# Kernel tuning notes

Measured on AMD Instinct MI355X. Metric: run time of the kernel, lower is better.

The kernel has to match this reference:

```python
import jax, jax.numpy as jnp
import numpy as np

#   x_out = Dy(alpha) @ J @ Dy(beta) @ J @ Dy(gamma) @ x   (per-irrep block diagonal)
# Dy(theta) is the sparse cos/sin y-rotation (exactly what encode_rotation_angle feeds
# into the segmented tensor product), and J = D(rotation by pi about (x+y)/sqrt(2)) is
# the constant Wigner matrix that conjugates a y-rotation into an x-rotation.

LMAX = 8
MUL = 64
LS = list(range(LMAX + 1))
DIM = MUL * sum(2 * l + 1 for l in LS)  # 5184
BATCH = 16384


def _so3_generators(l):
    # real antisymmetric so(3) generators for degree l (e3nn/cuE convention)
    m = np.arange(-l, l)
    raising = np.diag(-np.sqrt(l * (l + 1) - m * (m + 1)), k=-1).astype(np.complex128)
    m = np.arange(-l + 1, l + 1)
    lowering = np.diag(np.sqrt(l * (l + 1) - m * (m - 1)), k=1).astype(np.complex128)
    m = np.arange(-l, l + 1)
    X = np.stack([0.5 * (raising + lowering), np.diag(1j * m).astype(np.complex128),
                  -0.5j * (raising - lowering)])
    # change of basis complex -> real spherical harmonics
    q = np.zeros((2 * l + 1, 2 * l + 1), dtype=np.complex128)
    for mm in range(-l, 0):
        q[l + mm, l + abs(mm)] = 1.0 / np.sqrt(2)
        q[l + mm, l - abs(mm)] = -1j / np.sqrt(2)
    q[l, l] = 1.0
    for mm in range(1, l + 1):
        q[l + mm, l + abs(mm)] = (-1.0) ** mm / np.sqrt(2)
        q[l + mm, l - abs(mm)] = 1j * (-1.0) ** mm / np.sqrt(2)
    q = (-1j) ** l * q
    X = np.conj(q.T)[None] @ X @ q[None]
    return np.real(X)  # (3, 2l+1, 2l+1)


def _expm(A):
    w, V = np.linalg.eig(A.astype(np.complex128))
    return np.real(V @ np.diag(np.exp(w)) @ np.linalg.inv(V))


_J, _FREQ = [], []
for _l in LS:
    _X = _so3_generators(_l)
    # J = expm(pi * (Xx + Xy)/sqrt(2)): involution with J Dy(b) J = Dx(b)
    _J.append(jnp.asarray(_expm((np.pi / np.sqrt(2.0)) * (_X[0] + _X[1])), dtype=jnp.float32))
    _d = 2 * _l + 1
    # antidiagonal of the y-generator gives the per-row trig frequencies (+/- m)
    _FREQ.append(jnp.asarray(_X[1][np.arange(_d), _d - 1 - np.arange(_d)], dtype=jnp.float32))


def _rot_y(theta, freq, seg):
    # theta: [B], freq: [d], seg: [B, d, mul] (ir_mul layout)
    ang = freq * theta[:, None]                      # [B, d]
    return jnp.cos(ang)[..., None] * seg + jnp.sin(ang)[..., None] * seg[:, ::-1, :]


def setup_inputs() -> dict:
    key = jax.random.key(0)
    kg, kb, ka, kx = jax.random.split(key, 4)
    pi = float(np.pi)
    return {
        "gamma": jax.random.uniform(kg, (BATCH,), jnp.float32, -pi, pi),
        "beta": jax.random.uniform(kb, (BATCH,), jnp.float32, -pi, pi),
        "alpha": jax.random.uniform(ka, (BATCH,), jnp.float32, -pi, pi),
        "x": jax.random.normal(kx, (BATCH, DIM), jnp.float32),
    }


def reference(gamma, beta, alpha, x):
    outs = []
    off = 0
    for l, J, freq in zip(LS, _J, _FREQ):
        d = 2 * l + 1
        seg = x[:, off:off + d * MUL].reshape(-1, d, MUL)  # [B, 2l+1, mul]
        off += d * MUL
        seg = _rot_y(gamma, freq, seg)                      # first rotation about y
        seg = jnp.einsum('ij,bjm->bim', J, seg)
        seg = _rot_y(beta, freq, seg)                       # rotation about x (J-conjugated)
        seg = jnp.einsum('ij,bjm->bim', J, seg)
        seg = _rot_y(alpha, freq, seg)                      # last rotation about y
        outs.append(seg.reshape(-1, d * MUL))
    return jnp.concatenate(outs, axis=1)
```

## Files before the change

### kernel.cpp

```cpp
#include <hip/hip_runtime.h>
#include <math.h>
#include <complex>


#define LMAX 8
#define BATCH 16384
#define DIM 5184
#define NJ 969
#define NP 1140

__host__ __device__ constexpr int d_of(int l) { return 2 * l + 1; }
__host__ __device__ constexpr int joff_u(int l) {
    int o = 0;
    for (int k = 0; k < l; ++k) o += d_of(k) * d_of(k);
    return o;
}
__host__ __device__ constexpr int rp_of(int l) { return (d_of(l) + 3) & ~3; }
__host__ __device__ constexpr int poff_u(int l) {
    int o = 0;
    for (int k = 0; k < l; ++k) o += d_of(k) * rp_of(k);
    return o;
}

struct JPack { float v[NJ]; };

static void compute_J_host(JPack* jp) {
    for (int l = 0; l <= LMAX; ++l) {
        const int d = 2 * l + 1;
        std::complex<double> q[289], Ac[289], T1[289];
        double A[289], E[289], Tm[289], P[289];
        const double is2 = 1.0 / std::sqrt(2.0);
        static const double pr[4] = {1.0, 0.0, -1.0, 0.0};
        static const double pim[4] = {0.0, -1.0, 0.0, 1.0};
        const int ph = l & 3;
        for (int i = 0; i < d; ++i) {
            for (int j = 0; j < d; ++j) {
                double re = 0.0, im = 0.0;
                const int mm = i - l;
                if (mm < 0) {
                    if (j == l - mm) re = is2;
                    if (j == l + mm) im = -is2;
                } else if (mm == 0) {
                    if (j == l) re = 1.0;
                } else {
                    const double sgn = (mm & 1) ? -1.0 : 1.0;
                    if (j == l + mm) re = sgn * is2;
                    if (j == l - mm) im = sgn * is2;
                }
                q[i * d + j] = std::complex<double>(re * pr[ph] - im * pim[ph],
                                                    re * pim[ph] + im * pr[ph]);
                double xr = 0.0;
                if (j == i - 1) {
                    const double m = (double)(i - 1 - l);
                    xr += -0.5 * std::sqrt((double)l * (l + 1) - m * (m + 1));
                }
                if (j == i + 1) {
                    const double m = (double)(i - l + 1);
                    xr += 0.5 * std::sqrt((double)l * (l + 1) - m * (m - 1));
                }
                Ac[i * d + j] = std::complex<double>(xr, (i == j) ? (double)(i - l) : 0.0);
            }
        }
        for (int i = 0; i < d; ++i)
            for (int j = 0; j < d; ++j) {
                std::complex<double> s = 0.0;
                for (int k = 0; k < d; ++k) s += Ac[i * d + k] * q[k * d + j];
                T1[i * d + j] = s;
            }
        for (int i = 0; i < d; ++i)
            for (int j = 0; j < d; ++j) {
                std::complex<double> s = 0.0;
                for (int k = 0; k < d; ++k) s += std::conj(q[k * d + i]) * T1[k * d + j];
                A[i * d + j] = s.real() * (M_PI / std::sqrt(2.0));
            }
        double mx = 0.0;
        for (int i = 0; i < d; ++i) {
            double s = 0.0;
            for (int k = 0; k < d; ++k) s += std::fabs(A[i * d + k]);
            mx = std::fmax(mx, s);
        }
        int sh = 0;
        while (mx > 0.25 && sh < 60) { mx *= 0.5; ++sh; }
        const double sc = std::ldexp(1.0, -sh);
        for (int t = 0; t < d * d; ++t) A[t] *= sc;
        for (int i = 0; i < d; ++i)
            for (int j = 0; j < d; ++j) E[i * d + j] = Tm[i * d + j] = (i == j) ? 1.0 : 0.0;
        for (int kk = 1; kk <= 16; ++kk) {
            for (int i = 0; i < d; ++i)
                for (int j = 0; j < d; ++j) {
                    double s = 0.0;
                    for (int k = 0; k < d; ++k) s += Tm[i * d + k] * A[k * d + j];
                    P[i * d + j] = s / (double)kk;
                }
            for (int t = 0; t < d * d; ++t) { Tm[t] = P[t]; E[t] += P[t]; }
        }
        for (int q2 = 0; q2 < sh; ++q2) {
            for (int i = 0; i < d; ++i)
                for (int j = 0; j < d; ++j) {
                    double s = 0.0;
                    for (int k = 0; k < d; ++k) s += E[i * d + k] * E[k * d + j];
                    P[i * d + j] = s;
                }
            for (int t = 0; t < d * d; ++t) E[t] = P[t];
        }
        for (int i = 0; i < d; ++i)
            for (int j = 0; j < d; ++j)
                jp->v[joff_u(l) + i * d + j] = (float)E[i * d + j];
    }
}

template <int L>
__device__ __forceinline__ void compose(const float* __restrict__ sJ,
                                        float* __restrict__ Pw,
                                        float* __restrict__ Dw,
                                        const float (&T)[3][2][17],
                                        int lane) {
    constexpr int d = d_of(L), h = (d + 1) / 2, RP = rp_of(L);
    const float* J = sJ + joff_u(L);
    float* D = Dw + poff_u(L);
    for (int t = lane; t < h * d; t += 64) {
        const int i = t / d, j = t - i * d;
        const int i2 = d - 1 - i, j2 = d - 1 - j;
        const float cg = T[0][0][(L - j) + 8], sg = T[0][1][(L - j) + 8];
        const float p1a = J[i * d + j] * cg - J[i * d + j2] * sg;
        const float p1b = J[i2 * d + j] * cg - J[i2 * d + j2] * sg;
        const float cb = T[1][0][(L - i) + 8], sb = T[1][1][(L - i) + 8];
        Pw[i * d + j]  = cb * p1a + sb * p1b;
        Pw[i2 * d + j] = cb * p1b - sb * p1a;
    }
    __syncthreads();
    for (int t = lane; t < h * d; t += 64) {
        const int i = t / d, j = t - i * d;
        const int i2 = d - 1 - i;
        float ta = 0.f, tb = 0.f;
#pragma unroll
        for (int k = 0; k < d; ++k) {
            const float p = Pw[k * d + j];
            ta += J[i * d + k] * p;
            tb += J[i2 * d + k] * p;
        }
        const float ca = T[2][0][(L - i) + 8], sa = T[2][1][(L - i) + 8];
        D[i * RP + j]  = ca * ta + sa * tb;
        D[i2 * RP + j] = ca * tb - sa * ta;
    }
    __syncthreads();
}

template <int L>
__device__ __forceinline__ void apply(const float* __restrict__ xb,
                                      float* __restrict__ ob,
                                      const float* __restrict__ Dw) {
    constexpr int d = d_of(L), RP = rp_of(L);
    const float* __restrict__ D = Dw + poff_u(L);
    const float* p = xb + 64 * L * L;
    float* o = ob + 64 * L * L;
    float A[d];
#pragma unroll
    for (int i = 0; i < d; ++i) A[i] = p[i * 64];
#pragma unroll
    for (int i = 0; i < d; ++i) {
        const float4* row = reinterpret_cast<const float4*>(D + i * RP);
        float acc = 0.f;
#pragma unroll
        for (int q = 0; q < RP / 4; ++q) {
            const float4 f = row[q];
            if (4 * q + 0 < d) acc += f.x * A[4 * q + 0];
            if (4 * q + 1 < d) acc += f.y * A[4 * q + 1];
            if (4 * q + 2 < d) acc += f.z * A[4 * q + 2];
            if (4 * q + 3 < d) acc += f.w * A[4 * q + 3];
        }
        __builtin_nontemporal_store(acc, o + i * 64);
    }
}

__global__ __launch_bounds__(256) void rot_main(const float* __restrict__ gamma,
                                                const float* __restrict__ beta,
                                                const float* __restrict__ alpha,
                                                const float* __restrict__ x,
                                                float* __restrict__ out,
                                                const float* __restrict__ Jg) {
    __shared__ float sJ[NJ];
    __shared__ __align__(16) float sD[4][NP];
    __shared__ float sP[4][289];
    __shared__ float sT[4][3][2][17];

    const int tid = threadIdx.x;
    const int wave = tid >> 6, lane = tid & 63;
    const int b = blockIdx.x * 4 + wave;

    for (int i = tid; i < NJ; i += 256) sJ[i] = Jg[i];

    if (lane < 51) {
        const int a = lane / 17, mm = lane - a * 17;
        const float th = (a == 0) ? gamma[b] : ((a == 1) ? beta[b] : alpha[b]);
        float s, c;
        __sincosf((float)(mm - 8) * th, &s, &c);
        sT[wave][a][0][mm] = c;
        sT[wave][a][1][mm] = s;
    }
    __syncthreads();

    const float (&T)[3][2][17] = sT[wave];
    float* Pw = sP[wave];
    float* Dw = sD[wave];

    compose<0>(sJ, Pw, Dw, T, lane);
    compose<1>(sJ, Pw, Dw, T, lane);
    compose<2>(sJ, Pw, Dw, T, lane);
    compose<3>(sJ, Pw, Dw, T, lane);
    compose<4>(sJ, Pw, Dw, T, lane);
    compose<5>(sJ, Pw, Dw, T, lane);
    compose<6>(sJ, Pw, Dw, T, lane);
    compose<7>(sJ, Pw, Dw, T, lane);
    compose<8>(sJ, Pw, Dw, T, lane);

    const float* xb = x + (size_t)b * DIM + lane;
    float* ob = out + (size_t)b * DIM + lane;

    apply<0>(xb, ob, Dw);
    apply<1>(xb, ob, Dw);
    apply<2>(xb, ob, Dw);
    apply<3>(xb, ob, Dw);
    apply<4>(xb, ob, Dw);
    apply<5>(xb, ob, Dw);
    apply<6>(xb, ob, Dw);
    apply<7>(xb, ob, Dw);
    apply<8>(xb, ob, Dw);
}

extern "C" void kernel_launch(void* const* d_in, const int* in_sizes, int n_in,
                              void* d_out, int out_size, void* d_ws, size_t ws_size,
                              hipStream_t stream) {
    const float* gamma = (const float*)d_in[0];
    const float* beta  = (const float*)d_in[1];
    const float* alpha = (const float*)d_in[2];
    const float* x     = (const float*)d_in[3];
    float* out = (float*)d_out;

    static JPack jp;
    static bool init = false;
    if (!init) { compute_J_host(&jp); init = true; }

    hipMemcpyAsync(d_ws, jp.v, sizeof(JPack), hipMemcpyHostToDevice, stream);

    hipLaunchKernelGGL(rot_main, dim3(BATCH / 4), dim3(256), 0, stream,
                       gamma, beta, alpha, x, out, (const float*)d_ws);
}
```

Baseline: 149.2 us.

## Interleave per-degree compose with apply and use wave-local LDS fences

Merges the per-degree Wigner matrix composition and its application into one routine, issuing the global loads of x for each degree before the composition work so the memory latency hides behind the LDS math. Block-wide __syncthreads are replaced by a wave-local lgkmcnt wait, since each wave only touches its own scratch. The separate P scratch buffer is dropped and aliased into unused parts of the D buffer, with degrees processed from 8 down to 0 so the aliased space is not yet written. This lowers LDS footprint and may raise occupancy, but it depends on the alias offsets being correct and on the wave-local fence being a sufficient barrier.

```diff
diff --git a/kernel.cpp b/kernel.cpp
--- a/kernel.cpp
+++ b/kernel.cpp
@@ -109,15 +109,29 @@
     }
 }
 
-template <int L>
-__device__ __forceinline__ void compose(const float* __restrict__ sJ,
-                                        float* __restrict__ Pw,
-                                        float* __restrict__ Dw,
+__device__ __forceinline__ void wave_lds_fence() {
+    asm volatile("s_waitcnt lgkmcnt(0)" ::: "memory");
+    __builtin_amdgcn_sched_barrier(0);
+}
+
+template <int L, int PWOFF>
+__device__ __forceinline__ void process(const float* __restrict__ xb,
+                                        float* __restrict__ ob,
+                                        const float* __restrict__ sJ,
+                                        float* Dw,
                                         const float (&T)[3][2][17],
                                         int lane) {
     constexpr int d = d_of(L), h = (d + 1) / 2, RP = rp_of(L);
     const float* J = sJ + joff_u(L);
     float* D = Dw + poff_u(L);
+    float* Pw = Dw + PWOFF;
+    const float* p = xb + 64 * L * L;
+    float* o = ob + 64 * L * L;
+
+    float A[d];
+#pragma unroll
+    for (int i = 0; i < d; ++i) A[i] = p[i * 64];
+
     for (int t = lane; t < h * d; t += 64) {
         const int i = t / d, j = t - i * d;
         const int i2 = d - 1 - i, j2 = d - 1 - j;
@@ -128,35 +142,24 @@
         Pw[i * d + j]  = cb * p1a + sb * p1b;
         Pw[i2 * d + j] = cb * p1b - sb * p1a;
     }
-    __syncthreads();
+    wave_lds_fence();
+
     for (int t = lane; t < h * d; t += 64) {
         const int i = t / d, j = t - i * d;
         const int i2 = d - 1 - i;
         float ta = 0.f, tb = 0.f;
 #pragma unroll
         for (int k = 0; k < d; ++k) {
-            const float p = Pw[k * d + j];
-            ta += J[i * d + k] * p;
-            tb += J[i2 * d + k] * p;
+            const float pv = Pw[k * d + j];
+            ta += J[i * d + k] * pv;
+            tb += J[i2 * d + k] * pv;
         }
         const float ca = T[2][0][(L - i) + 8], sa = T[2][1][(L - i) + 8];
         D[i * RP + j]  = ca * ta + sa * tb;
         D[i2 * RP + j] = ca * tb - sa * ta;
     }
-    __syncthreads();
-}
-
-template <int L>
-__device__ __forceinline__ void apply(const float* __restrict__ xb,
-                                      float* __restrict__ ob,
-                                      const float* __restrict__ Dw) {
-    constexpr int d = d_of(L), RP = rp_of(L);
-    const float* __restrict__ D = Dw + poff_u(L);
-    const float* p = xb + 64 * L * L;
-    float* o = ob + 64 * L * L;
-    float A[d];
-#pragma unroll
-    for (int i = 0; i < d; ++i) A[i] = p[i * 64];
+    wave_lds_fence();
+
 #pragma unroll
     for (int i = 0; i < d; ++i) {
         const float4* row = reinterpret_cast<const float4*>(D + i * RP);
@@ -181,7 +184,6 @@
                                                 const float* __restrict__ Jg) {
     __shared__ float sJ[NJ];
     __shared__ __align__(16) float sD[4][NP];
-    __shared__ float sP[4][289];
     __shared__ float sT[4][3][2][17];
 
     const int tid = threadIdx.x;
@@ -201,31 +203,20 @@
     __syncthreads();
 
     const float (&T)[3][2][17] = sT[wave];
-    float* Pw = sP[wave];
     float* Dw = sD[wave];
-
-    compose<0>(sJ, Pw, Dw, T, lane);
-    compose<1>(sJ, Pw, Dw, T, lane);
-    compose<2>(sJ, Pw, Dw, T, lane);
-    compose<3>(sJ, Pw, Dw, T, lane);
-    compose<4>(sJ, Pw, Dw, T, lane);
-    compose<5>(sJ, Pw, Dw, T, lane);
-    compose<6>(sJ, Pw, Dw, T, lane);
-    compose<7>(sJ, Pw, Dw, T, lane);
-    compose<8>(sJ, Pw, Dw, T, lane);
 
     const float* xb = x + (size_t)b * DIM + lane;
     float* ob = out + (size_t)b * DIM + lane;
 
-    apply<0>(xb, ob, Dw);
-    apply<1>(xb, ob, Dw);
-    apply<2>(xb, ob, Dw);
-    apply<3>(xb, ob, Dw);
-    apply<4>(xb, ob, Dw);
-    apply<5>(xb, ob, Dw);
-    apply<6>(xb, ob, Dw);
-    apply<7>(xb, ob, Dw);
-    apply<8>(xb, ob, Dw);
+    process<8, 0>(xb, ob, sJ, Dw, T, lane);
+    process<7, 800>(xb, ob, sJ, Dw, T, lane);
+    process<6, 800>(xb, ob, sJ, Dw, T, lane);
+    process<5, 800>(xb, ob, sJ, Dw, T, lane);
+    process<4, 800>(xb, ob, sJ, Dw, T, lane);
+    process<3, 800>(xb, ob, sJ, Dw, T, lane);
+    process<2, 800>(xb, ob, sJ, Dw, T, lane);
+    process<1, 800>(xb, ob, sJ, Dw, T, lane);
+    process<0, 800>(xb, ob, sJ, Dw, T, lane);
 }
 
 extern "C" void kernel_launch(void* const* d_in, const int* in_sizes, int n_in,
```

After: 141.0 us. 1.06x faster.
